# Kernel optimization log

Measured on AMD Instinct MI355X. Metric: run time of the kernel, lower is better.

## Reference

```python
import jax, jax.numpy as jnp
import numpy as np

B, N, K = 8, 2048, 100  # graphs per batch, nodes per graph, diffpool clusters


def _bn(x, g, b, eps=1e-5):
    # BatchNorm1d in training mode over all B*N nodes (biased variance)
    m = x.mean(axis=(0, 1))
    v = x.var(axis=(0, 1))
    return (x - m) * jax.lax.rsqrt(v + eps) * g + b


def _norm_adj(A):
    # PyG gcn_norm: add remaining self-loops (fill=1), D^-1/2 (A+I) D^-1/2
    n = A.shape[-1]
    d = jnp.diagonal(A, axis1=-2, axis2=-1)
    A_hat = A + jnp.where(d == 0, 1.0, 0.0)[..., :, None] * jnp.eye(n, dtype=A.dtype)
    deg = A_hat.sum(-1)
    dinv = jnp.where(deg > 0, 1.0 / jnp.sqrt(deg), 0.0)
    return dinv[..., :, None] * A_hat * dinv[..., None, :]


def _gcn(An, x, W, b):
    # GCNConv: propagate(x @ W) + bias, with pre-normalized adjacency
    return An @ (x @ W) + b


def _forward(x, adj, W_in, W3030, Wp13, b30, b100, Wfc_pool, bfc_pool,
             W1, b1, W2, b2, gamma30, beta30, gamma100, beta100):
    A_w = _norm_adj(adj)                               # weighted (edge_attr) adjacency
    A_b = _norm_adj((adj > 0).astype(adj.dtype))       # pool convs ignore edge_attr
    # feature branch
    x11 = _bn(_gcn(A_w, x, W_in[0], b30[0]), gamma30[0], beta30[0])
    x12 = _bn(_gcn(A_w, x11, W3030[0], b30[1]), gamma30[1], beta30[1])
    x13 = _bn(_gcn(A_w, x12, W3030[1], b30[2]), gamma30[2], beta30[2])
    x1_out = jnp.concatenate([x11, x12, x13], -1).max(axis=1)   # [B,90]
    # assignment branch
    s11 = _bn(_gcn(A_b, x, W_in[1], b30[3]), gamma30[3], beta30[3])
    s12 = _bn(_gcn(A_b, s11, W3030[2], b30[4]), gamma30[4], beta30[4])
    s13 = _bn(_gcn(A_b, s12, Wp13, b100), gamma100, beta100)
    s1 = jnp.concatenate([s11, s12, s13], -1) @ Wfc_pool + bfc_pool  # [B,N,K]
    # dense_diff_pool (link/entropy losses are unused by the forward output)
    s = jax.nn.softmax(s1, -1)
    p1_x = jnp.einsum('bnk,bnd->bkd', s, x13)          # s^T x  [B,K,30]
    p1_adj = jnp.einsum('bnk,bnl->bkl', s, adj @ s)    # s^T A s  [B,K,K]
    # second stage on pooled (dense, weighted) graph
    A2 = _norm_adj(p1_adj)
    x21 = _bn(_gcn(A2, p1_x, W3030[3], b30[5]), gamma30[5], beta30[5])
    x22 = _bn(_gcn(A2, x21, W3030[4], b30[6]), gamma30[6], beta30[6])
    x23 = _bn(_gcn(A2, x22, W3030[5], b30[7]), gamma30[7], beta30[7])
    x2_out = jnp.concatenate([x21, x22, x23], -1).max(axis=1)   # [B,90]
    h = jnp.concatenate([x1_out, x2_out], -1) @ W1 + b1
    return jax.nn.relu(h) @ W2 + b2                    # [B,6]


def setup_inputs():
    key = jax.random.key(0)
    ks = jax.random.split(key, 12)
    u = jax.random.uniform(ks[0], (B, N, N), dtype=jnp.float32)
    mask = jax.random.uniform(ks[1], (B, N, N)) < 0.05
    A = jnp.triu(u * mask, 1)
    adj = A + jnp.swapaxes(A, -1, -2)
    x = jax.random.normal(ks[2], (B, N, 3), dtype=jnp.float32)
    w = lambda k, s: jax.random.normal(k, s, dtype=jnp.float32) * 0.1
    return dict(
        x=x, adj=adj,
        W_in=w(ks[3], (2, 3, 30)),      # conv11, pool_conv11
        W3030=w(ks[4], (6, 30, 30)),    # conv12, conv13, pool_conv12, conv21..23
        Wp13=w(ks[5], (30, 100)),
        b30=jnp.zeros((8, 30), jnp.float32),
        b100=jnp.zeros((100,), jnp.float32),
        Wfc_pool=w(ks[6], (160, 100)), bfc_pool=jnp.zeros((100,), jnp.float32),
        W1=w(ks[7], (180, 50)), b1=jnp.zeros((50,), jnp.float32),
        W2=w(ks[8], (50, 6)), b2=jnp.zeros((6,), jnp.float32),
        gamma30=jnp.ones((8, 30), jnp.float32), beta30=jnp.zeros((8, 30), jnp.float32),
        gamma100=jnp.ones((100,), jnp.float32), beta100=jnp.zeros((100,), jnp.float32),
    )


def reference(x, adj, W_in, W3030, Wp13, b30, b100, Wfc_pool, bfc_pool,
              W1, b1, W2, b2, gamma30, beta30, gamma100, beta100):
    return _forward(x, adj, W_in, W3030, Wp13, b30, b100, Wfc_pool, bfc_pool,
                    W1, b1, W2, b2, gamma30, beta30, gamma100, beta100)
```

## Files before the change

kernel.cpp:

```cpp
#include <hip/hip_runtime.h>
#include <hip/hip_fp16.h>
#include <cstdint>
#include <cstddef>

#define BATCH 8
#define NN 2048
#define RTOT 16384
#define CAP 176

static constexpr size_t OF_B1W   = 0;
static constexpr size_t OF_B1B   = 3840;
static constexpr size_t OF_B2W   = 7680;
static constexpr size_t OF_B2B   = 11520;
static constexpr size_t OF_B3W   = 15360;
static constexpr size_t OF_B3B   = 15840;
static constexpr size_t OF_S2    = 17440;
static constexpr size_t OF_CNT   = 17620;
static constexpr size_t ZEND     = 17632;
static constexpr size_t OF_ELLV  = 17664;
static constexpr size_t OF_ELLC  = OF_ELLV + 2883584;
static constexpr size_t OF_ROWLEN= OF_ELLC + 1441792;
static constexpr size_t OF_DINVW = OF_ROWLEN + 16384;
static constexpr size_t OF_DINVB = OF_DINVW + 16384;
static constexpr size_t OF_HWB   = OF_DINVB + 16384;
static constexpr size_t OF_HW3   = OF_HWB + 524288;
static constexpr size_t OF_HB100 = OF_HW3 + 262144;
static constexpr size_t OF_ZW    = OF_HB100 + 851968;
static constexpr size_t OF_ZB    = OF_ZW + 524288;
static constexpr size_t OF_X11   = OF_ZB + 1703936;
static constexpr size_t OF_X12   = OF_X11 + 524288;
static constexpr size_t OF_X13   = OF_X12 + 524288;
static constexpr size_t OF_S11   = OF_X13 + 524288;
static constexpr size_t OF_S12   = OF_S11 + 524288;
static constexpr size_t OF_PARTMAX = OF_S12 + 524288;
static constexpr size_t OF_PP    = OF_PARTMAX + 23040;
static constexpr size_t OF_PPOOL = OF_PP + 3328000;

#define FMA4(acc, s, h) { acc.x += (s)*(h).x; acc.y += (s)*(h).y; acc.z += (s)*(h).z; acc.w += (s)*(h).w; }

__device__ __forceinline__ unsigned short f2h(float f) {
  _Float16 h = (_Float16)f;
  return *(unsigned short*)&h;
}
__device__ __forceinline__ float h2f(unsigned short s) {
  _Float16 h = *(_Float16*)&s;
  return (float)h;
}
__device__ __forceinline__ float2 h2f2(unsigned int u) {
  __half2 h = *(__half2*)&u;
  return __half22float2(h);
}

struct __align__(8) us4 { unsigned short x, y, z, w; };

#define ACC8(g, wt) { \
  float2 f0=h2f2((g).x), f1=h2f2((g).y), f2=h2f2((g).z), f3=h2f2((g).w); \
  acc[0] += (wt)*f0.x; acc[1] += (wt)*f0.y; acc[2] += (wt)*f1.x; acc[3] += (wt)*f1.y; \
  acc[4] += (wt)*f2.x; acc[5] += (wt)*f2.y; acc[6] += (wt)*f3.x; acc[7] += (wt)*f3.y; }


__global__ __launch_bounds__(256) void k_build_ell(
    const float* __restrict__ adj, const float* __restrict__ x,
    const float* __restrict__ Win, float* __restrict__ ellv,
    unsigned short* __restrict__ ellc, int* __restrict__ rowlen,
    float* __restrict__ dinvw, float* __restrict__ dinvb,
    unsigned short* __restrict__ Hwb, float* __restrict__ zbase)
{
  int r = blockIdx.x;
  int t = threadIdx.x, lane = t & 63, wv = t >> 6;
  if (blockIdx.x < 69) {
    int zi = blockIdx.x * 256 + t;
    if (zi < (int)ZEND) zbase[zi] = 0.f;
  }
  const float* row = adj + (size_t)r * NN;
  __shared__ int wcnt[4];
  __shared__ float wsumA[4];
  __shared__ float dsh[2];
  float4 a = ((const float4*)row)[t];
  float4 b = ((const float4*)row)[256 + t];
  float vals[8] = {a.x, a.y, a.z, a.w, b.x, b.y, b.z, b.w};
  int cbase0 = t*4, cbase1 = 1024 + t*4;
  int cnt = 0; float sum = 0.f;
#pragma unroll
  for (int k = 0; k < 8; ++k) { sum += vals[k]; cnt += (vals[k] != 0.f) ? 1 : 0; }
  int pre = cnt;
#pragma unroll
  for (int o = 1; o < 64; o <<= 1) { int n = __shfl_up(pre, o); if (lane >= o) pre += n; }
  int excl = pre - cnt;
  int wtot = __shfl(pre, 63);
#pragma unroll
  for (int o = 32; o; o >>= 1) sum += __shfl_down(sum, o);
  if (lane == 0) { wcnt[wv] = wtot; wsumA[wv] = sum; }
  __syncthreads();
  int base = 0;
  for (int w = 0; w < wv; ++w) base += wcnt[w];
  int p = base + excl;
  size_t rb = (size_t)r * CAP;
#pragma unroll
  for (int k = 0; k < 8; ++k) {
    float v = vals[k];
    if (v != 0.f && p < CAP) {
      ellv[rb + p] = v;
      ellc[rb + p] = (unsigned short)((k < 4) ? (cbase0 + k) : (cbase1 + (k - 4)));
      ++p;
    }
  }
  if (t == 0) {
    int tot = wcnt[0] + wcnt[1] + wcnt[2] + wcnt[3];
    float ws = wsumA[0] + wsumA[1] + wsumA[2] + wsumA[3];
    int nnz = tot < CAP ? tot : CAP;
    int n = nnz;
    while ((n & 3) && n < CAP) { ellv[rb + n] = 0.f; ellc[rb + n] = 0; ++n; }
    rowlen[r] = n;
    float dw = rsqrtf(ws + 1.f), db = rsqrtf((float)nnz + 1.f);
    dinvw[r] = dw; dinvb[r] = db;
    dsh[0] = dw; dsh[1] = db;
  }
  __syncthreads();
  if (t < 64) {
    int c = t & 31, side = t >> 5;
    float v = 0.f;
    if (c < 30) {
      float x0 = x[r*3], x1 = x[r*3+1], x2 = x[r*3+2];
      const float* W = Win + side*90;
      v = (x0*W[c] + x1*W[30+c] + x2*W[60+c]) * dsh[side];
    }
    Hwb[(size_t)r*64 + t] = f2h(v);
  }
}

__global__ __launch_bounds__(256) void k_spmm_pair(
    const unsigned short* __restrict__ Hwb, const float* __restrict__ ellv,
    const unsigned short* __restrict__ ellc, const int* __restrict__ rowlen,
    const float* __restrict__ dinvw, const float* __restrict__ dinvb,
    float* __restrict__ Zw, float* __restrict__ Zb,
    float* __restrict__ bktW, float* __restrict__ bktB)
{
  __shared__ float zsW[32][32];
  __shared__ float zsB[32][32];
  int t = threadIdx.x;
  int gid = blockIdx.x * 256 + t;
  int row = gid >> 3, q = gid & 7;
  int side = q >> 2, sub = q & 3;
  int len = rowlen[row];
  const float4* ev = (const float4*)(ellv + (size_t)row * CAP);
  const uint2*  ec = (const uint2*) (ellc + (size_t)row * CAP);
  const uint4* HP = (const uint4*)(Hwb + (size_t)(row >> 11) * (NN*64));
  float acc[8] = {0,0,0,0,0,0,0,0};
  int nit = len >> 2;
  int i = 0;
  for (; i + 2 <= nit; i += 2) {
    float4 v0 = ev[i], v1 = ev[i+1];
    uint2 cc0 = ec[i], cc1 = ec[i+1];
    int a0 = cc0.x & 0xffff, a1 = cc0.x >> 16, a2 = cc0.y & 0xffff, a3 = cc0.y >> 16;
    int e0 = cc1.x & 0xffff, e1 = cc1.x >> 16, e2 = cc1.y & 0xffff, e3 = cc1.y >> 16;
    uint4 g0 = HP[a0*8+q], g1 = HP[a1*8+q], g2 = HP[a2*8+q], g3 = HP[a3*8+q];
    uint4 g4 = HP[e0*8+q], g5 = HP[e1*8+q], g6 = HP[e2*8+q], g7 = HP[e3*8+q];
    float w0 = side ? (v0.x>0.f?1.f:0.f) : v0.x;
    float w1 = side ? (v0.y>0.f?1.f:0.f) : v0.y;
    float w2 = side ? (v0.z>0.f?1.f:0.f) : v0.z;
    float w3 = side ? (v0.w>0.f?1.f:0.f) : v0.w;
    float w4 = side ? (v1.x>0.f?1.f:0.f) : v1.x;
    float w5 = side ? (v1.y>0.f?1.f:0.f) : v1.y;
    float w6 = side ? (v1.z>0.f?1.f:0.f) : v1.z;
    float w7 = side ? (v1.w>0.f?1.f:0.f) : v1.w;
    ACC8(g0, w0); ACC8(g1, w1); ACC8(g2, w2); ACC8(g3, w3);
    ACC8(g4, w4); ACC8(g5, w5); ACC8(g6, w6); ACC8(g7, w7);
  }
  if (i < nit) {
    float4 v = ev[i];
    uint2 cc = ec[i];
    int c0 = cc.x & 0xffff, c1 = cc.x >> 16, c2 = cc.y & 0xffff, c3 = cc.y >> 16;
    uint4 g0 = HP[c0*8+q], g1 = HP[c1*8+q], g2 = HP[c2*8+q], g3 = HP[c3*8+q];
    float w0 = side ? (v.x>0.f?1.f:0.f) : v.x;
    float w1 = side ? (v.y>0.f?1.f:0.f) : v.y;
    float w2 = side ? (v.z>0.f?1.f:0.f) : v.z;
    float w3 = side ? (v.w>0.f?1.f:0.f) : v.w;
    ACC8(g0, w0); ACC8(g1, w1); ACC8(g2, w2); ACC8(g3, w3);
  }
  uint4 hs = HP[(row & (NN-1))*8 + q];
  ACC8(hs, 1.f);
  float d = side ? dinvb[row] : dinvw[row];
#pragma unroll
  for (int k = 0; k < 8; ++k) acc[k] *= d;
  float* Zp = (side ? Zb : Zw) + (size_t)row*32 + sub*8;
  float4 o0 = {acc[0],acc[1],acc[2],acc[3]}, o1 = {acc[4],acc[5],acc[6],acc[7]};
  ((float4*)Zp)[0] = o0; ((float4*)Zp)[1] = o1;
  int rowloc = t >> 3;
  float (*zs)[32] = side ? zsB : zsW;
#pragma unroll
  for (int k = 0; k < 8; ++k) zs[rowloc][sub*8+k] = acc[k];
  __syncthreads();
  int copy = blockIdx.x & 63;
  if (t < 30) {
    float s1 = 0.f, s2 = 0.f;
    for (int r = 0; r < 32; ++r) { float v = zsW[r][t]; s1 += v; s2 += v*v; }
    atomicAdd(&bktW[(t*64+copy)*2],   s1);
    atomicAdd(&bktW[(t*64+copy)*2+1], s2);
  } else if (t >= 64 && t < 94) {
    int c = t - 64;
    float s1 = 0.f, s2 = 0.f;
    for (int r = 0; r < 32; ++r) { float v = zsB[r][c]; s1 += v; s2 += v*v; }
    atomicAdd(&bktB[(c*64+copy)*2],   s1);
    atomicAdd(&bktB[(c*64+copy)*2+1], s2);
  }
}

__global__ __launch_bounds__(256) void k_spmm_l3(
    const unsigned short* __restrict__ Hw3, const unsigned short* __restrict__ Hb100,
    const float* __restrict__ ellv, const unsigned short* __restrict__ ellc,
    const int* __restrict__ rowlen, const float* __restrict__ dinvw,
    const float* __restrict__ dinvb, float* __restrict__ Zw, float* __restrict__ Zb,
    float* __restrict__ bktW3, float* __restrict__ bktB3)
{
  __shared__ float zs[64][32];
  __shared__ float st[200];
  int t = threadIdx.x;
  if (blockIdx.x < 256) {
    int gid = blockIdx.x * 256 + t;
    int row = gid >> 2, q = gid & 3;
    int len = rowlen[row];
    const float4* ev = (const float4*)(ellv + (size_t)row * CAP);
    const uint2*  ec = (const uint2*) (ellc + (size_t)row * CAP);
    const uint4* HP = (const uint4*)(Hw3 + (size_t)(row >> 11) * (NN*32));
    float acc[8] = {0,0,0,0,0,0,0,0};
    int nit = len >> 2;
    int i = 0;
    for (; i + 2 <= nit; i += 2) {
      float4 v0 = ev[i], v1 = ev[i+1];
      uint2 cc0 = ec[i], cc1 = ec[i+1];
      int a0 = cc0.x & 0xffff, a1 = cc0.x >> 16, a2 = cc0.y & 0xffff, a3 = cc0.y >> 16;
      int e0 = cc1.x & 0xffff, e1 = cc1.x >> 16, e2 = cc1.y & 0xffff, e3 = cc1.y >> 16;
      uint4 g0 = HP[a0*4+q], g1 = HP[a1*4+q], g2 = HP[a2*4+q], g3 = HP[a3*4+q];
      uint4 g4 = HP[e0*4+q], g5 = HP[e1*4+q], g6 = HP[e2*4+q], g7 = HP[e3*4+q];
      ACC8(g0, v0.x); ACC8(g1, v0.y); ACC8(g2, v0.z); ACC8(g3, v0.w);
      ACC8(g4, v1.x); ACC8(g5, v1.y); ACC8(g6, v1.z); ACC8(g7, v1.w);
    }
    if (i < nit) {
      float4 v = ev[i];
      uint2 cc = ec[i];
      int c0 = cc.x & 0xffff, c1 = cc.x >> 16, c2 = cc.y & 0xffff, c3 = cc.y >> 16;
      uint4 g0 = HP[c0*4+q], g1 = HP[c1*4+q], g2 = HP[c2*4+q], g3 = HP[c3*4+q];
      ACC8(g0, v.x); ACC8(g1, v.y); ACC8(g2, v.z); ACC8(g3, v.w);
    }
    uint4 hs = HP[(row & (NN-1))*4 + q];
    ACC8(hs, 1.f);
    float d = dinvw[row];
#pragma unroll
    for (int k = 0; k < 8; ++k) acc[k] *= d;
    float* Zp = Zw + (size_t)row*32 + q*8;
    float4 o0 = {acc[0],acc[1],acc[2],acc[3]}, o1 = {acc[4],acc[5],acc[6],acc[7]};
    ((float4*)Zp)[0] = o0; ((float4*)Zp)[1] = o1;
    int rowloc = t >> 2;
#pragma unroll
    for (int k = 0; k < 8; ++k) zs[rowloc][q*8+k] = acc[k];
    __syncthreads();
    if (t < 30) {
      float s1 = 0.f, s2 = 0.f;
      for (int r = 0; r < 64; ++r) { float v = zs[r][t]; s1 += v; s2 += v*v; }
      int copy = blockIdx.x & 7;
      atomicAdd(&bktW3[(t*8+copy)*2],   s1);
      atomicAdd(&bktW3[(t*8+copy)*2+1], s2);
    }
  } else {
    int bid = blockIdx.x - 256;
    for (int i = t; i < 200; i += 256) st[i] = 0.f;
    __syncthreads();
    int gid = bid * 256 + t;
    int row = gid / 13, q = gid - row*13;
    int len = rowlen[row];
    const float4* ev = (const float4*)(ellv + (size_t)row * CAP);
    const uint2*  ec = (const uint2*) (ellc + (size_t)row * CAP);
    const uint4* HP = (const uint4*)(Hb100 + (size_t)(row >> 11) * ((size_t)NN*104));
    float acc[8] = {0,0,0,0,0,0,0,0};
    int nit = len >> 2;
    int i = 0;
    for (; i + 2 <= nit; i += 2) {
      float4 v0 = ev[i], v1 = ev[i+1];
      uint2 cc0 = ec[i], cc1 = ec[i+1];
      int a0 = cc0.x & 0xffff, a1 = cc0.x >> 16, a2 = cc0.y & 0xffff, a3 = cc0.y >> 16;
      int e0 = cc1.x & 0xffff, e1 = cc1.x >> 16, e2 = cc1.y & 0xffff, e3 = cc1.y >> 16;
      uint4 g0 = HP[a0*13+q], g1 = HP[a1*13+q], g2 = HP[a2*13+q], g3 = HP[a3*13+q];
      uint4 g4 = HP[e0*13+q], g5 = HP[e1*13+q], g6 = HP[e2*13+q], g7 = HP[e3*13+q];
      float w0 = (v0.x>0.f?1.f:0.f), w1 = (v0.y>0.f?1.f:0.f);
      float w2 = (v0.z>0.f?1.f:0.f), w3 = (v0.w>0.f?1.f:0.f);
      float w4 = (v1.x>0.f?1.f:0.f), w5 = (v1.y>0.f?1.f:0.f);
      float w6 = (v1.z>0.f?1.f:0.f), w7 = (v1.w>0.f?1.f:0.f);
      ACC8(g0, w0); ACC8(g1, w1); ACC8(g2, w2); ACC8(g3, w3);
      ACC8(g4, w4); ACC8(g5, w5); ACC8(g6, w6); ACC8(g7, w7);
    }
    if (i < nit) {
      float4 v = ev[i];
      uint2 cc = ec[i];
      int c0 = cc.x & 0xffff, c1 = cc.x >> 16, c2 = cc.y & 0xffff, c3 = cc.y >> 16;
      uint4 g0 = HP[c0*13+q], g1 = HP[c1*13+q], g2 = HP[c2*13+q], g3 = HP[c3*13+q];
      float w0 = (v.x>0.f?1.f:0.f), w1 = (v.y>0.f?1.f:0.f);
      float w2 = (v.z>0.f?1.f:0.f), w3 = (v.w>0.f?1.f:0.f);
      ACC8(g0, w0); ACC8(g1, w1); ACC8(g2, w2); ACC8(g3, w3);
    }
    uint4 hs = HP[(row & (NN-1))*13 + q];
    ACC8(hs, 1.f);
    float d = dinvb[row];
#pragma unroll
    for (int k = 0; k < 8; ++k) acc[k] *= d;
    float* Zp = Zb + (size_t)row*104 + q*8;
    float4 o0 = {acc[0],acc[1],acc[2],acc[3]}, o1 = {acc[4],acc[5],acc[6],acc[7]};
    ((float4*)Zp)[0] = o0; ((float4*)Zp)[1] = o1;
    int c0 = q*8;
#pragma unroll
    for (int k = 0; k < 8; ++k) {
      int ch = c0 + k;
      if (ch < 100) { atomicAdd(&st[ch*2], acc[k]); atomicAdd(&st[ch*2+1], acc[k]*acc[k]); }
    }
    __syncthreads();
    int copy = bid & 7;
    for (int i2 = t; i2 < 200; i2 += 256)
      atomicAdd(&bktB3[((i2>>1)*8 + copy)*2 + (i2&1)], st[i2]);
  }
}

template<int LEVEL>
__global__ __launch_bounds__(256) void k_apply_gemm(
    const float* __restrict__ Zw, const float* __restrict__ bktW,
    const float* __restrict__ gW, const float* __restrict__ beW,
    float* __restrict__ xst, const float* __restrict__ Ww,
    const float* __restrict__ dinvw,
    const float* __restrict__ Zb, const float* __restrict__ bktB,
    const float* __restrict__ gB, const float* __restrict__ beB,
    float* __restrict__ sst, const float* __restrict__ Wb,
    const float* __restrict__ dinvb,
    unsigned short* __restrict__ HwOut, unsigned short* __restrict__ HbOut)
{
  constexpr int NGB = (LEVEL == 1) ? 8 : 26;
  constexpr int OSTRIDEB = (LEVEL == 1) ? 32 : 104;
  constexpr int NG = 8 + NGB;
  __shared__ float WwL[30*32];
  __shared__ float WbL[30*OSTRIDEB];
  __shared__ float awL[60], abL[60];
  int t = threadIdx.x;
  if (t < 60) {
    int c = t % 30;
    bool isW = t < 30;
    const float4* p = (const float4*)((isW ? bktW : bktB) + c*128);
    float s1 = 0.f, s2 = 0.f;
#pragma unroll
    for (int k = 0; k < 32; ++k) { float4 v = p[k]; s1 += v.x + v.z; s2 += v.y + v.w; }
    float mean = s1/16384.f, var = s2/16384.f - mean*mean, inv = rsqrtf(var + 1e-5f);
    float aa = (isW ? gW : gB)[c]*inv;
    float* dst = isW ? awL : abL;
    dst[c] = aa; dst[30+c] = (isW ? beW : beB)[c] - mean*aa;
// ... 140 lines not shown
#pragma unroll
      for (int j = 0; j < 13; ++j) {
        if (j < klen) {
          float w = Wl[kk*100 + kbase + j];
          a0[j] += f0*w; a1[j] += f1*w;
        }
      }
    }
  }
  __syncthreads();
  float* sRow = shm;
  for (int j = 0; j < klen; ++j) {
    int k = kbase + j;
    sRow[n0*100 + k] = a0[j] + bfc[k];
    sRow[n1*100 + k] = a1[j] + bfc[k];
  }
  __syncthreads();
  int n = t >> 2, part = t & 3;
  int i0 = part*25;
  float m = -3.4e38f;
  for (int i = 0; i < 25; ++i) m = fmaxf(m, sRow[n*100 + i0 + i]);
  m = fmaxf(m, __shfl_xor(m, 1));
  m = fmaxf(m, __shfl_xor(m, 2));
  float ev[25]; float s = 0.f;
  for (int i = 0; i < 25; ++i) { float e = __expf(sRow[n*100 + i0 + i] - m); ev[i] = e; s += e; }
  s += __shfl_xor(s, 1);
  s += __shfl_xor(s, 2);
  float rinv = 1.f / s;
  for (int i = 0; i < 25; ++i) S[(size_t)(g0+n)*104 + i0 + i] = f2h(ev[i] * rinv);
  if (part == 3) {
    S[(size_t)(g0+n)*104 + 100] = 0; S[(size_t)(g0+n)*104 + 101] = 0;
    S[(size_t)(g0+n)*104 + 102] = 0; S[(size_t)(g0+n)*104 + 103] = 0;
  }
}

__global__ __launch_bounds__(256) void k_spmm_as(
    const unsigned short* __restrict__ S, const float* __restrict__ ellv,
    const unsigned short* __restrict__ ellc, const int* __restrict__ rowlen,
    float* __restrict__ Z)
{
  int t = threadIdx.x;
  int gid = blockIdx.x * 256 + t;
  int row = gid / 13, q = gid - row*13;
  int len = rowlen[row];
  const float4* ev = (const float4*)(ellv + (size_t)row * CAP);
  const uint2*  ec = (const uint2*) (ellc + (size_t)row * CAP);
  const uint4* HP = (const uint4*)(S + (size_t)(row >> 11) * ((size_t)NN*104));
  float acc[8] = {0,0,0,0,0,0,0,0};
  int nit = len >> 2;
  int i = 0;
  for (; i + 2 <= nit; i += 2) {
    float4 v0 = ev[i], v1 = ev[i+1];
    uint2 cc0 = ec[i], cc1 = ec[i+1];
    int a0 = cc0.x & 0xffff, a1 = cc0.x >> 16, a2 = cc0.y & 0xffff, a3 = cc0.y >> 16;
    int e0 = cc1.x & 0xffff, e1 = cc1.x >> 16, e2 = cc1.y & 0xffff, e3 = cc1.y >> 16;
    uint4 g0 = HP[a0*13+q], g1 = HP[a1*13+q], g2 = HP[a2*13+q], g3 = HP[a3*13+q];
    uint4 g4 = HP[e0*13+q], g5 = HP[e1*13+q], g6 = HP[e2*13+q], g7 = HP[e3*13+q];
    ACC8(g0, v0.x); ACC8(g1, v0.y); ACC8(g2, v0.z); ACC8(g3, v0.w);
    ACC8(g4, v1.x); ACC8(g5, v1.y); ACC8(g6, v1.z); ACC8(g7, v1.w);
  }
  if (i < nit) {
    float4 v = ev[i];
    uint2 cc = ec[i];
    int c0 = cc.x & 0xffff, c1 = cc.x >> 16, c2 = cc.y & 0xffff, c3 = cc.y >> 16;
    uint4 g0 = HP[c0*13+q], g1 = HP[c1*13+q], g2 = HP[c2*13+q], g3 = HP[c3*13+q];
    ACC8(g0, v.x); ACC8(g1, v.y); ACC8(g2, v.z); ACC8(g3, v.w);
  }
  float* Zp = Z + (size_t)row*104 + q*8;
  float4 o0 = {acc[0],acc[1],acc[2],acc[3]}, o1 = {acc[4],acc[5],acc[6],acc[7]};
  ((float4*)Zp)[0] = o0; ((float4*)Zp)[1] = o1;
}

__global__ __launch_bounds__(256) void k_pool_part(
    const unsigned short* __restrict__ S, const float* __restrict__ x13,
    const float* __restrict__ As, const float* __restrict__ x11,
    const float* __restrict__ x12, float* __restrict__ pp, float* __restrict__ pm)
{
  __shared__ float sL[64][100];
  __shared__ float xL[64][132];
  __shared__ float red[256];
  int t = threadIdx.x;
  int b = blockIdx.x >> 5, chunk = blockIdx.x & 31;
  int g0 = b * 2048 + chunk * 64;
  int kt = t/10, dt = t%10;
  int k0 = kt*4, d0 = dt*13;
  float acc[4][13];
#pragma unroll
  for (int a = 0; a < 4; ++a)
#pragma unroll
    for (int j = 0; j < 13; ++j) acc[a][j] = 0.f;
  for (int idx = t; idx < 64*100; idx += 256) {
    int l = idx/100, k = idx%100;
    sL[l][k] = h2f(S[(size_t)(g0+l)*104 + k]);
  }
  for (int idx = t; idx < 64*130; idx += 256) {
    int l = idx/130, d = idx%130;
    xL[l][d] = d < 30 ? x13[(size_t)(g0+l)*32 + d] : As[(size_t)(g0+l)*104 + (d-30)];
  }
  __syncthreads();
  if (t < 250) {
    for (int kk = 0; kk < 64; ++kk) {
      float sv[4];
#pragma unroll
// ... 195 lines not shown
    float a = b2[t];
    for (int j = 0; j < 50; ++j) a += hh[j]*W2[j*6+t];
    out[b*6+t] = a;
  }
}

extern "C" void kernel_launch(void* const* d_in, const int* in_sizes, int n_in,
                              void* d_out, int out_size, void* d_ws, size_t ws_size,
                              hipStream_t stream)
{
  const float* x    = (const float*)d_in[0];
  const float* adj  = (const float*)d_in[1];
  const float* Win  = (const float*)d_in[2];
  const float* W3030= (const float*)d_in[3];
  const float* Wp13 = (const float*)d_in[4];
  const float* Wfc  = (const float*)d_in[7];
  const float* bfc  = (const float*)d_in[8];
  const float* W1   = (const float*)d_in[9];
  const float* b1   = (const float*)d_in[10];
  const float* W2   = (const float*)d_in[11];
  const float* b2   = (const float*)d_in[12];
  const float* g30  = (const float*)d_in[13];
  const float* be30 = (const float*)d_in[14];
  const float* g100 = (const float*)d_in[15];
  const float* be100= (const float*)d_in[16];
  float* out = (float*)d_out;

  float* wsf = (float*)d_ws;
  float* bL1W = wsf + OF_B1W;  float* bL1B = wsf + OF_B1B;
  float* bL2W = wsf + OF_B2W;  float* bL2B = wsf + OF_B2B;
  float* bL3W = wsf + OF_B3W;  float* bL3B = wsf + OF_B3B;
  float* bktS2 = wsf + OF_S2;
  int*   cnt  = (int*)(wsf + OF_CNT);
  float* ellv  = wsf + OF_ELLV;
  unsigned short* ellc = (unsigned short*)(wsf + OF_ELLC);
  int*   rowlen = (int*)(wsf + OF_ROWLEN);
  float* dinvw = wsf + OF_DINVW;
  float* dinvb = wsf + OF_DINVB;
  unsigned short* Hwb   = (unsigned short*)(wsf + OF_HWB);
  unsigned short* Hw3   = (unsigned short*)(wsf + OF_HW3);
  unsigned short* Hb100 = (unsigned short*)(wsf + OF_HB100);
  unsigned short* S     = Hb100;
  float* Zw = wsf + OF_ZW;
  float* Zb = wsf + OF_ZB;
  float* x11 = wsf + OF_X11;
  float* x12 = wsf + OF_X12;
  float* x13 = wsf + OF_X13;
  float* s11 = wsf + OF_S11;
  float* s12 = wsf + OF_S12;
  float* pp  = wsf + OF_PP;
  float* ppool = wsf + OF_PPOOL;
  float* partmax = wsf + OF_PARTMAX;

  k_build_ell<<<RTOT, 256, 0, stream>>>(adj, x, Win, ellv, ellc, rowlen, dinvw, dinvb, Hwb, wsf);

  k_spmm_pair<<<512, 256, 0, stream>>>(Hwb, ellv, ellc, rowlen, dinvw, dinvb, Zw, Zb, bL1W, bL1B);
  k_apply_gemm<1><<<1024, 256, 0, stream>>>(Zw, bL1W, g30+0, be30+0, x11, W3030+0, dinvw,
                                            Zb, bL1B, g30+90, be30+90, s11, W3030+2*900, dinvb, Hwb, Hwb);

  k_spmm_pair<<<512, 256, 0, stream>>>(Hwb, ellv, ellc, rowlen, dinvw, dinvb, Zw, Zb, bL2W, bL2B);
  k_apply_gemm<2><<<2176, 256, 0, stream>>>(Zw, bL2W, g30+30, be30+30, x12, W3030+900, dinvw,
                                            Zb, bL2B, g30+120, be30+120, s12, Wp13, dinvb, Hw3, Hb100);

  k_spmm_l3<<<1088, 256, 0, stream>>>(Hw3, Hb100, ellv, ellc, rowlen, dinvw, dinvb, Zw, Zb, bL3W, bL3B);
  k_fcpool<<<256, 256, 0, stream>>>(Zw, bL3W, g30+60, be30+60, Zb, bL3B, g100, be100,
                                    s11, s12, Wfc, bfc, x13, S);

  k_spmm_as<<<832, 256, 0, stream>>>(S, ellv, ellc, rowlen, Zb );
  k_pool_part<<<256, 256, 0, stream>>>(S, x13, Zb, x11, x12, pp, partmax);
  k_pool_reduce<<<408, 256, 0, stream>>>(pp, ppool);

  k_s2fused<<<BATCH, 256, 0, stream>>>(ppool, partmax, W3030+3*900, g30+150, be30+150,
                                       bktS2, cnt, W1, b1, W2, b2, out);
}
```

Measured before the change: 549.0 us.

## Replace ELL sparse propagation with dense fp16 MFMA GEMMs over adjacency

Drops the ELL sparse format and builds dense fp16 copies of the weighted and binary adjacency, self-loop diagonal included. All graph propagations (pair layers, layer 3, and A·S) become dense GEMMs using 16x16x32 f16 MFMA instructions, with the feature operand staged through shared memory. This removes irregular gather traffic and the neighbour-count cap, but does about 20x more arithmetic on a ~5% dense matrix. It also reads 2×64 MB of fp16 adjacency per layer and rounds edge weights to fp16.

```diff
diff --git a/kernel.cpp b/kernel.cpp
--- a/kernel.cpp
+++ b/kernel.cpp
@@ -6,7 +6,6 @@
 #define BATCH 8
 #define NN 2048
 #define RTOT 16384
-#define CAP 176
 
 static constexpr size_t OF_B1W   = 0;
 static constexpr size_t OF_B1B   = 3840;
@@ -17,10 +16,7 @@
 static constexpr size_t OF_S2    = 17440;
 static constexpr size_t OF_CNT   = 17620;
 static constexpr size_t ZEND     = 17632;
-static constexpr size_t OF_ELLV  = 17664;
-static constexpr size_t OF_ELLC  = OF_ELLV + 2883584;
-static constexpr size_t OF_ROWLEN= OF_ELLC + 1441792;
-static constexpr size_t OF_DINVW = OF_ROWLEN + 16384;
+static constexpr size_t OF_DINVW = 17664;
 static constexpr size_t OF_DINVB = OF_DINVW + 16384;
 static constexpr size_t OF_HWB   = OF_DINVB + 16384;
 static constexpr size_t OF_HW3   = OF_HWB + 524288;
@@ -35,6 +31,11 @@
 static constexpr size_t OF_PARTMAX = OF_S12 + 524288;
 static constexpr size_t OF_PP    = OF_PARTMAX + 23040;
 static constexpr size_t OF_PPOOL = OF_PP + 3328000;
+static constexpr size_t OF_AW    = OF_PPOOL + 104000;
+static constexpr size_t OF_AB    = OF_AW + 16777216;
+
+typedef _Float16 f16x8 __attribute__((ext_vector_type(8)));
+typedef float f32x4 __attribute__((ext_vector_type(4)));
 
 #define FMA4(acc, s, h) { acc.x += (s)*(h).x; acc.y += (s)*(h).y; acc.z += (s)*(h).z; acc.w += (s)*(h).w; }
 
@@ -46,23 +47,14 @@
   _Float16 h = *(_Float16*)&s;
   return (float)h;
 }
-__device__ __forceinline__ float2 h2f2(unsigned int u) {
-  __half2 h = *(__half2*)&u;
-  return __half22float2(h);
-}
 
 struct __align__(8) us4 { unsigned short x, y, z, w; };
 
-#define ACC8(g, wt) { \
-  float2 f0=h2f2((g).x), f1=h2f2((g).y), f2=h2f2((g).z), f3=h2f2((g).w); \
-  acc[0] += (wt)*f0.x; acc[1] += (wt)*f0.y; acc[2] += (wt)*f1.x; acc[3] += (wt)*f1.y; \
-  acc[4] += (wt)*f2.x; acc[5] += (wt)*f2.y; acc[6] += (wt)*f3.x; acc[7] += (wt)*f3.y; }
-
-
-__global__ __launch_bounds__(256) void k_build_ell(
+
+__global__ __launch_bounds__(256) void k_build(
     const float* __restrict__ adj, const float* __restrict__ x,
-    const float* __restrict__ Win, float* __restrict__ ellv,
-    unsigned short* __restrict__ ellc, int* __restrict__ rowlen,
+    const float* __restrict__ Win,
+    _Float16* __restrict__ Aw, _Float16* __restrict__ Ab,
     float* __restrict__ dinvw, float* __restrict__ dinvb,
     unsigned short* __restrict__ Hwb, float* __restrict__ zbase)
 {
@@ -76,43 +68,33 @@
   __shared__ int wcnt[4];
   __shared__ float wsumA[4];
   __shared__ float dsh[2];
-  float4 a = ((const float4*)row)[t];
-  float4 b = ((const float4*)row)[256 + t];
+  float4 a = ((const float4*)row)[2*t];
+  float4 b = ((const float4*)row)[2*t + 1];
   float vals[8] = {a.x, a.y, a.z, a.w, b.x, b.y, b.z, b.w};
-  int cbase0 = t*4, cbase1 = 1024 + t*4;
+  int cbase = t << 3;
+  int rloc = r & (NN-1);
   int cnt = 0; float sum = 0.f;
 #pragma unroll
   for (int k = 0; k < 8; ++k) { sum += vals[k]; cnt += (vals[k] != 0.f) ? 1 : 0; }
-  int pre = cnt;
-#pragma unroll
-  for (int o = 1; o < 64; o <<= 1) { int n = __shfl_up(pre, o); if (lane >= o) pre += n; }
-  int excl = pre - cnt;
-  int wtot = __shfl(pre, 63);
-#pragma unroll
-  for (int o = 32; o; o >>= 1) sum += __shfl_down(sum, o);
-  if (lane == 0) { wcnt[wv] = wtot; wsumA[wv] = sum; }
-  __syncthreads();
-  int base = 0;
-  for (int w = 0; w < wv; ++w) base += wcnt[w];
-  int p = base + excl;
-  size_t rb = (size_t)r * CAP;
+#pragma unroll
+  for (int o = 32; o; o >>= 1) { sum += __shfl_down(sum, o); cnt += __shfl_down(cnt, o); }
+  if (lane == 0) { wcnt[wv] = cnt; wsumA[wv] = sum; }
+  f16x8 wv8, bv8;
 #pragma unroll
   for (int k = 0; k < 8; ++k) {
+    int c = cbase + k;
     float v = vals[k];
-    if (v != 0.f && p < CAP) {
-      ellv[rb + p] = v;
-      ellc[rb + p] = (unsigned short)((k < 4) ? (cbase0 + k) : (cbase1 + (k - 4)));
-      ++p;
-    }
-  }
+    bool dg = (c == rloc);
+    wv8[k] = (_Float16)(dg ? 1.f : v);
+    bv8[k] = (_Float16)((dg || v != 0.f) ? 1.f : 0.f);
+  }
+  *(f16x8*)(Aw + ((size_t)r << 11) + cbase) = wv8;
+  *(f16x8*)(Ab + ((size_t)r << 11) + cbase) = bv8;
+  __syncthreads();
   if (t == 0) {
     int tot = wcnt[0] + wcnt[1] + wcnt[2] + wcnt[3];
     float ws = wsumA[0] + wsumA[1] + wsumA[2] + wsumA[3];
-    int nnz = tot < CAP ? tot : CAP;
-    int n = nnz;
-    while ((n & 3) && n < CAP) { ellv[rb + n] = 0.f; ellc[rb + n] = 0; ++n; }
-    rowlen[r] = n;
-    float dw = rsqrtf(ws + 1.f), db = rsqrtf((float)nnz + 1.f);
+    float dw = rsqrtf(ws + 1.f), db = rsqrtf((float)tot + 1.f);
     dinvw[r] = dw; dinvb[r] = db;
     dsh[0] = dw; dsh[1] = db;
   }
@@ -129,131 +111,119 @@
   }
 }
 
-__global__ __launch_bounds__(256) void k_spmm_pair(
-    const unsigned short* __restrict__ Hwb, const float* __restrict__ ellv,
-    const unsigned short* __restrict__ ellc, const int* __restrict__ rowlen,
+__global__ __launch_bounds__(256) void k_gemm_pair(
+    const _Float16* __restrict__ Aw, const _Float16* __restrict__ Ab,
+    const unsigned short* __restrict__ H,
     const float* __restrict__ dinvw, const float* __restrict__ dinvb,
     float* __restrict__ Zw, float* __restrict__ Zb,
     float* __restrict__ bktW, float* __restrict__ bktB)
 {
-  __shared__ float zsW[32][32];
-  __shared__ float zsB[32][32];
+  __shared__ unsigned short BT[32][72];
+  __shared__ float zs[64][32];
   int t = threadIdx.x;
-  int gid = blockIdx.x * 256 + t;
-  int row = gid >> 3, q = gid & 7;
-  int side = q >> 2, sub = q & 3;
-  int len = rowlen[row];
-  const float4* ev = (const float4*)(ellv + (size_t)row * CAP);
-  const uint2*  ec = (const uint2*) (ellc + (size_t)row * CAP);
-  const uint4* HP = (const uint4*)(Hwb + (size_t)(row >> 11) * (NN*64));
-  float acc[8] = {0,0,0,0,0,0,0,0};
-  int nit = len >> 2;
-  int i = 0;
-  for (; i + 2 <= nit; i += 2) {
-    float4 v0 = ev[i], v1 = ev[i+1];
-    uint2 cc0 = ec[i], cc1 = ec[i+1];
-    int a0 = cc0.x & 0xffff, a1 = cc0.x >> 16, a2 = cc0.y & 0xffff, a3 = cc0.y >> 16;
-    int e0 = cc1.x & 0xffff, e1 = cc1.x >> 16, e2 = cc1.y & 0xffff, e3 = cc1.y >> 16;
-    uint4 g0 = HP[a0*8+q], g1 = HP[a1*8+q], g2 = HP[a2*8+q], g3 = HP[a3*8+q];
-    uint4 g4 = HP[e0*8+q], g5 = HP[e1*8+q], g6 = HP[e2*8+q], g7 = HP[e3*8+q];
-    float w0 = side ? (v0.x>0.f?1.f:0.f) : v0.x;
-    float w1 = side ? (v0.y>0.f?1.f:0.f) : v0.y;
-    float w2 = side ? (v0.z>0.f?1.f:0.f) : v0.z;
-    float w3 = side ? (v0.w>0.f?1.f:0.f) : v0.w;
-    float w4 = side ? (v1.x>0.f?1.f:0.f) : v1.x;
-    float w5 = side ? (v1.y>0.f?1.f:0.f) : v1.y;
-    float w6 = side ? (v1.z>0.f?1.f:0.f) : v1.z;
-    float w7 = side ? (v1.w>0.f?1.f:0.f) : v1.w;
-    ACC8(g0, w0); ACC8(g1, w1); ACC8(g2, w2); ACC8(g3, w3);
-    ACC8(g4, w4); ACC8(g5, w5); ACC8(g6, w6); ACC8(g7, w7);
-  }
-  if (i < nit) {
-    float4 v = ev[i];
-    uint2 cc = ec[i];
-    int c0 = cc.x & 0xffff, c1 = cc.x >> 16, c2 = cc.y & 0xffff, c3 = cc.y >> 16;
-    uint4 g0 = HP[c0*8+q], g1 = HP[c1*8+q], g2 = HP[c2*8+q], g3 = HP[c3*8+q];
-    float w0 = side ? (v.x>0.f?1.f:0.f) : v.x;
-    float w1 = side ? (v.y>0.f?1.f:0.f) : v.y;
-    float w2 = side ? (v.z>0.f?1.f:0.f) : v.z;
-    float w3 = side ? (v.w>0.f?1.f:0.f) : v.w;
-    ACC8(g0, w0); ACC8(g1, w1); ACC8(g2, w2); ACC8(g3, w3);
-  }
-  uint4 hs = HP[(row & (NN-1))*8 + q];
-  ACC8(hs, 1.f);
-  float d = side ? dinvb[row] : dinvw[row];
-#pragma unroll
-  for (int k = 0; k < 8; ++k) acc[k] *= d;
-  float* Zp = (side ? Zb : Zw) + (size_t)row*32 + sub*8;
-  float4 o0 = {acc[0],acc[1],acc[2],acc[3]}, o1 = {acc[4],acc[5],acc[6],acc[7]};
-  ((float4*)Zp)[0] = o0; ((float4*)Zp)[1] = o1;
-  int rowloc = t >> 3;
-  float (*zs)[32] = side ? zsB : zsW;
-#pragma unroll
-  for (int k = 0; k < 8; ++k) zs[rowloc][sub*8+k] = acc[k];
+  int side = blockIdx.x >> 8;
+  int mb = blockIdx.x & 255;
+  int row0 = mb << 6;
+  int g = row0 >> 11;
+  int w = t >> 6, l = t & 63, lc = l & 15, kg = l >> 4;
+  const _Float16* A = side ? Ab : Aw;
+  const _Float16* Arow = A + ((size_t)(row0 + (w << 4) + lc) << 11);
+  int hr = t >> 2, hc = (t & 3) << 3;
+  const unsigned short* hbase = H + (((size_t)g << 11) << 6) + (side << 5) + hc;
+  f32x4 acc0 = {0,0,0,0}, acc1 = {0,0,0,0};
+  for (int k0 = 0; k0 < 2048; k0 += 64) {
+    __syncthreads();
+    uint4 hv = *(const uint4*)(hbase + ((size_t)(k0 + hr) << 6));
+    const unsigned short* pv = (const unsigned short*)&hv;
+#pragma unroll
+    for (int j = 0; j < 8; ++j) BT[hc + j][hr] = pv[j];
+    __syncthreads();
+#pragma unroll
+    for (int kk = 0; kk < 64; kk += 32) {
+      f16x8 af = *(const f16x8*)(Arow + k0 + kk + (kg << 3));
+      f16x8 b0 = *(const f16x8*)&BT[lc][kk + (kg << 3)];
+      f16x8 b1 = *(const f16x8*)&BT[16 + lc][kk + (kg << 3)];
+      acc0 = __builtin_amdgcn_mfma_f32_16x16x32_f16(af, b0, acc0, 0, 0, 0);
+      acc1 = __builtin_amdgcn_mfma_f32_16x16x32_f16(af, b1, acc1, 0, 0, 0);
+    }
+  }
+  int rb = (w << 4) + (kg << 2);
+#pragma unroll
+  for (int i = 0; i < 4; ++i) { zs[rb + i][lc] = acc0[i]; zs[rb + i][16 + lc] = acc1[i]; }
+  __syncthreads();
+  {
+    int r = t >> 2, c8 = (t & 3) << 3;
+    float d = (side ? dinvb : dinvw)[row0 + r];
+    float o[8];
+#pragma unroll
+    for (int j = 0; j < 8; ++j) o[j] = zs[r][c8 + j] * d;
+#pragma unroll
+    for (int j = 0; j < 8; ++j) zs[r][c8 + j] = o[j];
+    float* Zp = (side ? Zb : Zw) + (((size_t)(row0 + r)) << 5) + c8;
+    float4 o0 = {o[0],o[1],o[2],o[3]}, o1 = {o[4],o[5],o[6],o[7]};
+    ((float4*)Zp)[0] = o0; ((float4*)Zp)[1] = o1;
+  }
   __syncthreads();
   int copy = blockIdx.x & 63;
   if (t < 30) {
     float s1 = 0.f, s2 = 0.f;
-    for (int r = 0; r < 32; ++r) { float v = zsW[r][t]; s1 += v; s2 += v*v; }
-    atomicAdd(&bktW[(t*64+copy)*2],   s1);
-    atomicAdd(&bktW[(t*64+copy)*2+1], s2);
-  } else if (t >= 64 && t < 94) {
-    int c = t - 64;
-    float s1 = 0.f, s2 = 0.f;
-    for (int r = 0; r < 32; ++r) { float v = zsB[r][c]; s1 += v; s2 += v*v; }
-    atomicAdd(&bktB[(c*64+copy)*2],   s1);
-    atomicAdd(&bktB[(c*64+copy)*2+1], s2);
-  }
-}
-
-__global__ __launch_bounds__(256) void k_spmm_l3(
+    for (int r = 0; r < 64; ++r) { float v = zs[r][t]; s1 += v; s2 += v*v; }
+    float* bkt = side ? bktB : bktW;
+    atomicAdd(&bkt[(t*64+copy)*2],   s1);
+    atomicAdd(&bkt[(t*64+copy)*2+1], s2);
+  }
+}
+
+__global__ __launch_bounds__(256) void k_gemm_l3(
+    const _Float16* __restrict__ Aw, const _Float16* __restrict__ Ab,
     const unsigned short* __restrict__ Hw3, const unsigned short* __restrict__ Hb100,
-    const float* __restrict__ ellv, const unsigned short* __restrict__ ellc,
-    const int* __restrict__ rowlen, const float* __restrict__ dinvw,
-    const float* __restrict__ dinvb, float* __restrict__ Zw, float* __restrict__ Zb,
+    const float* __restrict__ dinvw, const float* __restrict__ dinvb,
+    float* __restrict__ Zw, float* __restrict__ Zb,
     float* __restrict__ bktW3, float* __restrict__ bktB3)
 {
-  __shared__ float zs[64][32];
-  __shared__ float st[200];
+  __shared__ unsigned short BT[112][72];
+  __shared__ float zsst[2048];
   int t = threadIdx.x;
+  int w = t >> 6, l = t & 63, lc = l & 15, kg = l >> 4;
   if (blockIdx.x < 256) {
-    int gid = blockIdx.x * 256 + t;
-    int row = gid >> 2, q = gid & 3;
-    int len = rowlen[row];
-    const float4* ev = (const float4*)(ellv + (size_t)row * CAP);
-    const uint2*  ec = (const uint2*) (ellc + (size_t)row * CAP);
-    const uint4* HP = (const uint4*)(Hw3 + (size_t)(row >> 11) * (NN*32));
-    float acc[8] = {0,0,0,0,0,0,0,0};
-    int nit = len >> 2;
-    int i = 0;
-    for (; i + 2 <= nit; i += 2) {
-      float4 v0 = ev[i], v1 = ev[i+1];
-      uint2 cc0 = ec[i], cc1 = ec[i+1];
-      int a0 = cc0.x & 0xffff, a1 = cc0.x >> 16, a2 = cc0.y & 0xffff, a3 = cc0.y >> 16;
-      int e0 = cc1.x & 0xffff, e1 = cc1.x >> 16, e2 = cc1.y & 0xffff, e3 = cc1.y >> 16;
-      uint4 g0 = HP[a0*4+q], g1 = HP[a1*4+q], g2 = HP[a2*4+q], g3 = HP[a3*4+q];
-      uint4 g4 = HP[e0*4+q], g5 = HP[e1*4+q], g6 = HP[e2*4+q], g7 = HP[e3*4+q];
-      ACC8(g0, v0.x); ACC8(g1, v0.y); ACC8(g2, v0.z); ACC8(g3, v0.w);
-      ACC8(g4, v1.x); ACC8(g5, v1.y); ACC8(g6, v1.z); ACC8(g7, v1.w);
-    }
-    if (i < nit) {
-      float4 v = ev[i];
-      uint2 cc = ec[i];
-      int c0 = cc.x & 0xffff, c1 = cc.x >> 16, c2 = cc.y & 0xffff, c3 = cc.y >> 16;
-      uint4 g0 = HP[c0*4+q], g1 = HP[c1*4+q], g2 = HP[c2*4+q], g3 = HP[c3*4+q];
-      ACC8(g0, v.x); ACC8(g1, v.y); ACC8(g2, v.z); ACC8(g3, v.w);
-    }
-    uint4 hs = HP[(row & (NN-1))*4 + q];
-    ACC8(hs, 1.f);
-    float d = dinvw[row];
-#pragma unroll
-    for (int k = 0; k < 8; ++k) acc[k] *= d;
-    float* Zp = Zw + (size_t)row*32 + q*8;
-    float4 o0 = {acc[0],acc[1],acc[2],acc[3]}, o1 = {acc[4],acc[5],acc[6],acc[7]};
-    ((float4*)Zp)[0] = o0; ((float4*)Zp)[1] = o1;
-    int rowloc = t >> 2;
-#pragma unroll
-    for (int k = 0; k < 8; ++k) zs[rowloc][q*8+k] = acc[k];
+    int row0 = blockIdx.x << 6, g = row0 >> 11;
+    const _Float16* Arow = Aw + ((size_t)(row0 + (w << 4) + lc) << 11);
+    int hr = t >> 2, hc = (t & 3) << 3;
+    const unsigned short* hbase = Hw3 + (((size_t)g << 11) << 5) + hc;
+    f32x4 acc0 = {0,0,0,0}, acc1 = {0,0,0,0};
+    for (int k0 = 0; k0 < 2048; k0 += 64) {
+      __syncthreads();
+      uint4 hv = *(const uint4*)(hbase + ((size_t)(k0 + hr) << 5));
+      const unsigned short* pv = (const unsigned short*)&hv;
+#pragma unroll
+      for (int j = 0; j < 8; ++j) BT[hc + j][hr] = pv[j];
+      __syncthreads();
+#pragma unroll
+      for (int kk = 0; kk < 64; kk += 32) {
+        f16x8 af = *(const f16x8*)(Arow + k0 + kk + (kg << 3));
+        f16x8 b0 = *(const f16x8*)&BT[lc][kk + (kg << 3)];
+        f16x8 b1 = *(const f16x8*)&BT[16 + lc][kk + (kg << 3)];
+        acc0 = __builtin_amdgcn_mfma_f32_16x16x32_f16(af, b0, acc0, 0, 0, 0);
+        acc1 = __builtin_amdgcn_mfma_f32_16x16x32_f16(af, b1, acc1, 0, 0, 0);
+      }
+    }
+    float (*zs)[32] = (float (*)[32])zsst;
+    int rb = (w << 4) + (kg << 2);
+#pragma unroll
+    for (int i = 0; i < 4; ++i) { zs[rb + i][lc] = acc0[i]; zs[rb + i][16 + lc] = acc1[i]; }
+    __syncthreads();
+    {
+      int r = t >> 2, c8 = (t & 3) << 3;
+      float d = dinvw[row0 + r];
+      float o[8];
+#pragma unroll
+      for (int j = 0; j < 8; ++j) o[j] = zs[r][c8 + j] * d;
+#pragma unroll
+      for (int j = 0; j < 8; ++j) zs[r][c8 + j] = o[j];
+      float* Zp = Zw + (((size_t)(row0 + r)) << 5) + c8;
+      float4 o0 = {o[0],o[1],o[2],o[3]}, o1 = {o[4],o[5],o[6],o[7]};
+      ((float4*)Zp)[0] = o0; ((float4*)Zp)[1] = o1;
+    }
     __syncthreads();
     if (t < 30) {
       float s1 = 0.f, s2 = 0.f;
@@ -263,59 +233,99 @@
       atomicAdd(&bktW3[(t*8+copy)*2+1], s2);
     }
   } else {
-    int bid = blockIdx.x - 256;
-    for (int i = t; i < 200; i += 256) st[i] = 0.f;
-    __syncthreads();
-    int gid = bid * 256 + t;
-    int row = gid / 13, q = gid - row*13;
-    int len = rowlen[row];
-    const float4* ev = (const float4*)(ellv + (size_t)row * CAP);
-    const uint2*  ec = (const uint2*) (ellc + (size_t)row * CAP);
-    const uint4* HP = (const uint4*)(Hb100 + (size_t)(row >> 11) * ((size_t)NN*104));
-    float acc[8] = {0,0,0,0,0,0,0,0};
-    int nit = len >> 2;
-    int i = 0;
-    for (; i + 2 <= nit; i += 2) {
-      float4 v0 = ev[i], v1 = ev[i+1];
-      uint2 cc0 = ec[i], cc1 = ec[i+1];
-      int a0 = cc0.x & 0xffff, a1 = cc0.x >> 16, a2 = cc0.y & 0xffff, a3 = cc0.y >> 16;
-      int e0 = cc1.x & 0xffff, e1 = cc1.x >> 16, e2 = cc1.y & 0xffff, e3 = cc1.y >> 16;
-      uint4 g0 = HP[a0*13+q], g1 = HP[a1*13+q], g2 = HP[a2*13+q], g3 = HP[a3*13+q];
-      uint4 g4 = HP[e0*13+q], g5 = HP[e1*13+q], g6 = HP[e2*13+q], g7 = HP[e3*13+q];
-      float w0 = (v0.x>0.f?1.f:0.f), w1 = (v0.y>0.f?1.f:0.f);
-      float w2 = (v0.z>0.f?1.f:0.f), w3 = (v0.w>0.f?1.f:0.f);
-      float w4 = (v1.x>0.f?1.f:0.f), w5 = (v1.y>0.f?1.f:0.f);
-      float w6 = (v1.z>0.f?1.f:0.f), w7 = (v1.w>0.f?1.f:0.f);
-      ACC8(g0, w0); ACC8(g1, w1); ACC8(g2, w2); ACC8(g3, w3);
-      ACC8(g4, w4); ACC8(g5, w5); ACC8(g6, w6); ACC8(g7, w7);
-    }
-    if (i < nit) {
-      float4 v = ev[i];
-      uint2 cc = ec[i];
-      int c0 = cc.x & 0xffff, c1 = cc.x >> 16, c2 = cc.y & 0xffff, c3 = cc.y >> 16;
-      uint4 g0 = HP[c0*13+q], g1 = HP[c1*13+q], g2 = HP[c2*13+q], g3 = HP[c3*13+q];
-      float w0 = (v.x>0.f?1.f:0.f), w1 = (v.y>0.f?1.f:0.f);
-      float w2 = (v.z>0.f?1.f:0.f), w3 = (v.w>0.f?1.f:0.f);
-      ACC8(g0, w0); ACC8(g1, w1); ACC8(g2, w2); ACC8(g3, w3);
-    }
-    uint4 hs = HP[(row & (NN-1))*13 + q];
-    ACC8(hs, 1.f);
-    float d = dinvb[row];
-#pragma unroll
-    for (int k = 0; k < 8; ++k) acc[k] *= d;
-    float* Zp = Zb + (size_t)row*104 + q*8;
-    float4 o0 = {acc[0],acc[1],acc[2],acc[3]}, o1 = {acc[4],acc[5],acc[6],acc[7]};
-    ((float4*)Zp)[0] = o0; ((float4*)Zp)[1] = o1;
-    int c0 = q*8;
-#pragma unroll
-    for (int k = 0; k < 8; ++k) {
-      int ch = c0 + k;
-      if (ch < 100) { atomicAdd(&st[ch*2], acc[k]); atomicAdd(&st[ch*2+1], acc[k]*acc[k]); }
-    }
-    __syncthreads();
-    int copy = bid & 7;
+    int row0 = (blockIdx.x - 256) << 6, g = row0 >> 11;
+    const _Float16* Arow = Ab + ((size_t)(row0 + (w << 4) + lc) << 11);
+    for (int s = t; s < 200; s += 256) zsst[s] = 0.f;
+    for (int s = t; s < 576; s += 256) BT[104 + s/72][s%72] = 0;
+    f32x4 acc[7];
+#pragma unroll
+    for (int f = 0; f < 7; ++f) acc[f] = (f32x4){0,0,0,0};
+    for (int k0 = 0; k0 < 2048; k0 += 64) {
+      __syncthreads();
+      for (int idx = t; idx < 832; idx += 256) {
+        int r = idx / 13, c8 = (idx - r*13) << 3;
+        const unsigned short* hp = Hb100 + (size_t)((g << 11) + k0 + r) * 104 + c8;
+        uint4 hv = *(const uint4*)hp;
+        const unsigned short* pv = (const unsigned short*)&hv;
+#pragma unroll
+        for (int j = 0; j < 8; ++j) BT[c8 + j][r] = pv[j];
+      }
+      __syncthreads();
+#pragma unroll
+      for (int kk = 0; kk < 64; kk += 32) {
+        f16x8 af = *(const f16x8*)(Arow + k0 + kk + (kg << 3));
+#pragma unroll
+        for (int f = 0; f < 7; ++f) {
+          f16x8 bf = *(const f16x8*)&BT[f*16 + lc][kk + (kg << 3)];
+          acc[f] = __builtin_amdgcn_mfma_f32_16x16x32_f16(af, bf, acc[f], 0, 0, 0);
+        }
+      }
+    }
+    int rb = (w << 4) + (kg << 2);
+    float d[4];
+#pragma unroll
+    for (int i = 0; i < 4; ++i) d[i] = dinvb[row0 + rb + i];
+#pragma unroll
+    for (int f = 0; f < 7; ++f) {
+      int col = f*16 + lc;
+#pragma unroll
+      for (int i = 0; i < 4; ++i) {
+        float v = acc[f][i] * d[i];
+        if (col < 104) Zb[(size_t)(row0 + rb + i) * 104 + col] = v;
+        if (col < 100) { atomicAdd(&zsst[col*2], v); atomicAdd(&zsst[col*2+1], v*v); }
+      }
+    }
+    __syncthreads();
+    int copy = blockIdx.x & 7;
     for (int i2 = t; i2 < 200; i2 += 256)
-      atomicAdd(&bktB3[((i2>>1)*8 + copy)*2 + (i2&1)], st[i2]);
+      atomicAdd(&bktB3[((i2>>1)*8 + copy)*2 + (i2&1)], zsst[i2]);
+  }
+}
+
+__global__ __launch_bounds__(256) void k_gemm_as(
+    const _Float16* __restrict__ Aw, const unsigned short* __restrict__ S,
+    float* __restrict__ As)
+{
+  __shared__ unsigned short BT[112][72];
+  int t = threadIdx.x;
+  int w = t >> 6, l = t & 63, lc = l & 15, kg = l >> 4;
+  int row0 = blockIdx.x << 6, g = row0 >> 11;
+  const _Float16* Arow = Aw + ((size_t)(row0 + (w << 4) + lc) << 11);
+  for (int s = t; s < 576; s += 256) BT[104 + s/72][s%72] = 0;
+  f32x4 acc[7];
+#pragma unroll
+  for (int f = 0; f < 7; ++f) acc[f] = (f32x4){0,0,0,0};
+  for (int k0 = 0; k0 < 2048; k0 += 64) {
+    __syncthreads();
+    for (int idx = t; idx < 832; idx += 256) {
+      int r = idx / 13, c8 = (idx - r*13) << 3;
+      const unsigned short* hp = S + (size_t)((g << 11) + k0 + r) * 104 + c8;
+      uint4 hv = *(const uint4*)hp;
+      const unsigned short* pv = (const unsigned short*)&hv;
+#pragma unroll
+      for (int j = 0; j < 8; ++j) BT[c8 + j][r] = pv[j];
+    }
+    __syncthreads();
+#pragma unroll
+    for (int kk = 0; kk < 64; kk += 32) {
+      f16x8 af = *(const f16x8*)(Arow + k0 + kk + (kg << 3));
+#pragma unroll
+      for (int f = 0; f < 7; ++f) {
+        f16x8 bf = *(const f16x8*)&BT[f*16 + lc][kk + (kg << 3)];
+        acc[f] = __builtin_amdgcn_mfma_f32_16x16x32_f16(af, bf, acc[f], 0, 0, 0);
+      }
+    }
+  }
+  int rb = (w << 4) + (kg << 2);
+#pragma unroll
+  for (int f = 0; f < 7; ++f) {
+    int col = f*16 + lc;
+#pragma unroll
+    for (int i = 0; i < 4; ++i) {
+      int row = row0 + rb + i;
+      if (col < 104)
+        As[(size_t)row * 104 + col] = acc[f][i] - h2f(S[(size_t)row * 104 + col]);
+    }
   }
 }
 
@@ -522,43 +532,6 @@
     S[(size_t)(g0+n)*104 + 100] = 0; S[(size_t)(g0+n)*104 + 101] = 0;
     S[(size_t)(g0+n)*104 + 102] = 0; S[(size_t)(g0+n)*104 + 103] = 0;
   }
-}
-
-__global__ __launch_bounds__(256) void k_spmm_as(
-    const unsigned short* __restrict__ S, const float* __restrict__ ellv,
-    const unsigned short* __restrict__ ellc, const int* __restrict__ rowlen,
-    float* __restrict__ Z)
-{
-  int t = threadIdx.x;
-  int gid = blockIdx.x * 256 + t;
-  int row = gid / 13, q = gid - row*13;
-  int len = rowlen[row];
-  const float4* ev = (const float4*)(ellv + (size_t)row * CAP);
-  const uint2*  ec = (const uint2*) (ellc + (size_t)row * CAP);
-  const uint4* HP = (const uint4*)(S + (size_t)(row >> 11) * ((size_t)NN*104));
-  float acc[8] = {0,0,0,0,0,0,0,0};
-  int nit = len >> 2;
-  int i = 0;
-  for (; i + 2 <= nit; i += 2) {
-    float4 v0 = ev[i], v1 = ev[i+1];
-    uint2 cc0 = ec[i], cc1 = ec[i+1];
-    int a0 = cc0.x & 0xffff, a1 = cc0.x >> 16, a2 = cc0.y & 0xffff, a3 = cc0.y >> 16;
-    int e0 = cc1.x & 0xffff, e1 = cc1.x >> 16, e2 = cc1.y & 0xffff, e3 = cc1.y >> 16;
-    uint4 g0 = HP[a0*13+q], g1 = HP[a1*13+q], g2 = HP[a2*13+q], g3 = HP[a3*13+q];
-    uint4 g4 = HP[e0*13+q], g5 = HP[e1*13+q], g6 = HP[e2*13+q], g7 = HP[e3*13+q];
-    ACC8(g0, v0.x); ACC8(g1, v0.y); ACC8(g2, v0.z); ACC8(g3, v0.w);
-    ACC8(g4, v1.x); ACC8(g5, v1.y); ACC8(g6, v1.z); ACC8(g7, v1.w);
-  }
-  if (i < nit) {
-    float4 v = ev[i];
-    uint2 cc = ec[i];
-    int c0 = cc.x & 0xffff, c1 = cc.x >> 16, c2 = cc.y & 0xffff, c3 = cc.y >> 16;
-    uint4 g0 = HP[c0*13+q], g1 = HP[c1*13+q], g2 = HP[c2*13+q], g3 = HP[c3*13+q];
-    ACC8(g0, v.x); ACC8(g1, v.y); ACC8(g2, v.z); ACC8(g3, v.w);
-  }
-  float* Zp = Z + (size_t)row*104 + q*8;
-  float4 o0 = {acc[0],acc[1],acc[2],acc[3]}, o1 = {acc[4],acc[5],acc[6],acc[7]};
-  ((float4*)Zp)[0] = o0; ((float4*)Zp)[1] = o1;
 }
 
 __global__ __launch_bounds__(256) void k_pool_part(
@@ -820,9 +793,6 @@
   float* bL3W = wsf + OF_B3W;  float* bL3B = wsf + OF_B3B;
   float* bktS2 = wsf + OF_S2;
   int*   cnt  = (int*)(wsf + OF_CNT);
-  float* ellv  = wsf + OF_ELLV;
-  unsigned short* ellc = (unsigned short*)(wsf + OF_ELLC);
-  int*   rowlen = (int*)(wsf + OF_ROWLEN);
   float* dinvw = wsf + OF_DINVW;
   float* dinvb = wsf + OF_DINVB;
   unsigned short* Hwb   = (unsigned short*)(wsf + OF_HWB);
@@ -839,22 +809,24 @@
   float* pp  = wsf + OF_PP;
   float* ppool = wsf + OF_PPOOL;
   float* partmax = wsf + OF_PARTMAX;
-
-  k_build_ell<<<RTOT, 256, 0, stream>>>(adj, x, Win, ellv, ellc, rowlen, dinvw, dinvb, Hwb, wsf);
-
-  k_spmm_pair<<<512, 256, 0, stream>>>(Hwb, ellv, ellc, rowlen, dinvw, dinvb, Zw, Zb, bL1W, bL1B);
+  _Float16* Aw = (_Float16*)(wsf + OF_AW);
+  _Float16* Ab = (_Float16*)(wsf + OF_AB);
+
+  k_build<<<RTOT, 256, 0, stream>>>(adj, x, Win, Aw, Ab, dinvw, dinvb, Hwb, wsf);
+
+  k_gemm_pair<<<512, 256, 0, stream>>>(Aw, Ab, Hwb, dinvw, dinvb, Zw, Zb, bL1W, bL1B);
   k_apply_gemm<1><<<1024, 256, 0, stream>>>(Zw, bL1W, g30+0, be30+0, x11, W3030+0, dinvw,
                                             Zb, bL1B, g30+90, be30+90, s11, W3030+2*900, dinvb, Hwb, Hwb);
 
-  k_spmm_pair<<<512, 256, 0, stream>>>(Hwb, ellv, ellc, rowlen, dinvw, dinvb, Zw, Zb, bL2W, bL2B);
+  k_gemm_pair<<<512, 256, 0, stream>>>(Aw, Ab, Hwb, dinvw, dinvb, Zw, Zb, bL2W, bL2B);
   k_apply_gemm<2><<<2176, 256, 0, stream>>>(Zw, bL2W, g30+30, be30+30, x12, W3030+900, dinvw,
                                             Zb, bL2B, g30+120, be30+120, s12, Wp13, dinvb, Hw3, Hb100);
 
-  k_spmm_l3<<<1088, 256, 0, stream>>>(Hw3, Hb100, ellv, ellc, rowlen, dinvw, dinvb, Zw, Zb, bL3W, bL3B);
+  k_gemm_l3<<<512, 256, 0, stream>>>(Aw, Ab, Hw3, Hb100, dinvw, dinvb, Zw, Zb, bL3W, bL3B);
   k_fcpool<<<256, 256, 0, stream>>>(Zw, bL3W, g30+60, be30+60, Zb, bL3B, g100, be100,
                                     s11, s12, Wfc, bfc, x13, S);
 
-  k_spmm_as<<<832, 256, 0, stream>>>(S, ellv, ellc, rowlen, Zb );
+  k_gemm_as<<<256, 256, 0, stream>>>(Aw, S, Zb );
   k_pool_part<<<256, 256, 0, stream>>>(S, x13, Zb, x11, x12, pp, partmax);
   k_pool_reduce<<<408, 256, 0, stream>>>(pp, ppool);
 
```

New measurement: 711.5 us. 1.3x slower.
